# Performance work log

Hardware: AMD Instinct MI355X
Metric: run time of the kernel (lower is better)

The kernel has to match this reference:

```python
import jax, jax.numpy as jnp
import numpy as np

EPS = 1e-5


def setup_inputs() -> dict:
    key = jax.random.key(0)
    ks = jax.random.split(key, 12)
    B, C, H, W = 32, 512, 32, 32
    Ci = C // 2
    s_in = 1.0 / np.sqrt(C)
    s_ci = 1.0 / np.sqrt(Ci)
    return {
        "x": jax.random.normal(ks[0], (B, C, H, W), jnp.float32),
        # 1x1 conv weights stored as [out, in]
        "Wg": jax.random.normal(ks[1], (Ci, C), jnp.float32) * s_in,
        "bg": jax.random.normal(ks[2], (Ci,), jnp.float32) * 0.01,
        "Wt": jax.random.normal(ks[3], (Ci, C), jnp.float32) * s_in,
        "bt": jax.random.normal(ks[4], (Ci,), jnp.float32) * 0.01,
        "Wp": jax.random.normal(ks[5], (Ci, C), jnp.float32) * s_in,
        "bp": jax.random.normal(ks[6], (Ci,), jnp.float32) * 0.01,
        "Wz": jax.random.normal(ks[7], (C, Ci), jnp.float32) * s_ci,
        "bz": jax.random.normal(ks[8], (C,), jnp.float32) * 0.01,
        # BN affine params (torch inits these to 0 but we use nonzero for a meaningful baseline)
        "gamma": jax.random.normal(ks[9], (C,), jnp.float32) * 0.1,
        "beta": jax.random.normal(ks[10], (C,), jnp.float32) * 0.1,
    }


def reference(x, Wg, bg, Wt, bt, Wp, bp, Wz, bz, gamma, beta):
    B, C, H, W = x.shape
    N = H * W
    xr = x.reshape(B, C, N)
    # 1x1 conv projections (pure channel GEMMs)
    g_x = jnp.einsum('oc,bcn->bno', Wg, xr) + bg            # [B,N,Ci]
    theta_x = jnp.einsum('oc,bcn->bno', Wt, xr) + bt        # [B,N,Ci]
    phi_x = jnp.einsum('oc,bcn->bon', Wp, xr) + bp[None, :, None]  # [B,Ci,N]
    # full non-local attention over all N=H*W positions
    f = jnp.einsum('bnc,bcm->bnm', theta_x, phi_x)          # [B,N,N]
    attn = jax.nn.softmax(f, axis=-1)
    y = jnp.einsum('bnm,bmo->bon', attn, g_x)               # [B,Ci,N]
    # output 1x1 conv
    w_y = jnp.einsum('oc,bcn->bon', Wz, y) + bz[None, :, None]  # [B,C,N]
    # BatchNorm2d (training mode: batch statistics over B and spatial dims)
    mean = jnp.mean(w_y, axis=(0, 2), keepdims=True)
    var = jnp.var(w_y, axis=(0, 2), keepdims=True)
    w_y = (w_y - mean) / jnp.sqrt(var + EPS)
    w_y = w_y * gamma[None, :, None] + beta[None, :, None]
    return w_y.reshape(B, C, H, W) + x
```

## Files before the change

### kernel.cpp

```cpp
#include <hip/hip_runtime.h>
#include <math.h>

typedef __bf16 bf16;
typedef __bf16 bf16x8 __attribute__((ext_vector_type(8)));
typedef float f32x4 __attribute__((ext_vector_type(4)));
typedef unsigned short u16;
typedef unsigned int u32;

constexpr int BATCH = 32;
constexpr int CH    = 512;
constexpr int CI    = 256;
constexpr int NSP   = 1024;
constexpr int OCH   = 768;
constexpr float EPSV = 1e-5f;

__device__ __forceinline__ void gload_lds16(const bf16* g, bf16* l) {
    __builtin_amdgcn_global_load_lds(
        (const __attribute__((address_space(1))) void*)g,
        (__attribute__((address_space(3))) void*)l, 16, 0, 0);
}

__global__ void prep_weights(const float* __restrict__ Wg, const float* __restrict__ Wt,
                             const float* __restrict__ Wp, const float* __restrict__ Wz,
                             bf16* __restrict__ wc, bf16* __restrict__ wz,
                             float* __restrict__ sums) {
    int tid = blockIdx.x * 256 + threadIdx.x;
    if (tid < 1024) sums[tid] = 0.0f;
    if (tid < OCH * CH) {
        int r = tid / CH, c = tid % CH;
        float v;
        if (r < 256)      v = Wt[r * CH + c];
        else if (r < 512) v = Wp[(r - 256) * CH + c];
        else              v = Wg[(r - 512) * CH + c];
        wc[(size_t)(c >> 6) * (OCH * 64) + r * 64 + (c & 63)] = (bf16)v;
    } else {
        int t2 = tid - OCH * CH;
        if (t2 < CH * CI) {
            int r = t2 / CI, o = t2 % CI;
            wz[(size_t)(o >> 6) * (CH * 64) + r * 64 + (o & 63)] = (bf16)Wz[r * CI + o];
        }
    }
}

__global__ void transpose_x(const float* __restrict__ x, bf16* __restrict__ xb) {
    __shared__ bf16 tile[64][64];
    int b = blockIdx.z, kt = blockIdx.y, nb = blockIdx.x;
    int t = threadIdx.x;
    {
        int c_loc = t >> 2;
        int nq = t & 3;
        const float* src = x + ((size_t)b * CH + kt * 64 + c_loc) * NSP + nb * 64 + nq * 16;
        float vv[16];
        *(float4*)(vv + 0)  = *(const float4*)(src + 0);
        *(float4*)(vv + 4)  = *(const float4*)(src + 4);
        *(float4*)(vv + 8)  = *(const float4*)(src + 8);
        *(float4*)(vv + 12) = *(const float4*)(src + 12);
        int nbase = nq * 16;
        #pragma unroll
        for (int i = 0; i < 16; ++i) tile[nbase + i][c_loc] = (bf16)vv[i];
    }
    __syncthreads();
    {
        int n_loc = t >> 2;
        int cq = t & 3;
        bf16* dst = xb + ((((size_t)b * 8 + kt) * NSP) + nb * 64 + n_loc) * 64 + cq * 16;
        *(uint4*)(dst)     = *(const uint4*)&tile[n_loc][cq * 16];
        *(uint4*)(dst + 8) = *(const uint4*)&tile[n_loc][cq * 16 + 8];
    }
}

__launch_bounds__(256, 2)
__global__ void proj_gemm(const bf16* __restrict__ xb, const bf16* __restrict__ wc,
                          const float* __restrict__ bt, const float* __restrict__ bp,
                          const float* __restrict__ bg,
                          bf16* __restrict__ theta, bf16* __restrict__ phi_t,
                          bf16* __restrict__ gt_t) {
    constexpr int LDA = 72;
    __shared__ __align__(16) bf16 sm[2 * 128 * LDA];
    bf16* As = sm;
    bf16* Bs = sm + 128 * LDA;
    int b = blockIdx.z;
    int n0 = blockIdx.y * 128;
    int oc0 = blockIdx.x * 128;
    int t = threadIdx.x, lane = t & 63, wid = t >> 6;
    int wm = wid >> 1, wn = wid & 1;
    int l15 = lane & 15, quad = lane >> 4;

    f32x4 acc[4][4] = {};
    for (int kt = 0; kt < 8; ++kt) {
        __syncthreads();
        const bf16* asrc = xb + ((((size_t)b * 8 + kt) * NSP) + n0) * 64;
        const bf16* bsrc = wc + ((size_t)kt * OCH + oc0) * 64;
        for (int s = t; s < 1024; s += 256) {
            int row = s >> 3, c8 = s & 7;
            *(uint4*)&As[row * LDA + c8 * 8] = *(const uint4*)(asrc + (size_t)s * 8);
            *(uint4*)&Bs[row * LDA + c8 * 8] = *(const uint4*)(bsrc + (size_t)s * 8);
        }
        __syncthreads();
        #pragma unroll
        for (int kc = 0; kc < 2; ++kc) {
            bf16x8 af[4], bfv[4];
            #pragma unroll
            for (int i = 0; i < 4; ++i) {
                af[i]  = *(const bf16x8*)&As[(wm * 64 + i * 16 + l15) * LDA + kc * 32 + quad * 8];
                bfv[i] = *(const bf16x8*)&Bs[(wn * 64 + i * 16 + l15) * LDA + kc * 32 + quad * 8];
            }
            #pragma unroll
            for (int i = 0; i < 4; ++i)
                #pragma unroll
                for (int j = 0; j < 4; ++j)
                    acc[i][j] = __builtin_amdgcn_mfma_f32_16x16x32_bf16(af[i], bfv[j], acc[i][j], 0, 0, 0);
        }
    }
    if (oc0 < 256) {
        #pragma unroll
        for (int j = 0; j < 4; ++j) {
            int och = oc0 + wn * 64 + j * 16 + l15;
            float bv = bt[och];
            #pragma unroll
            for (int i = 0; i < 4; ++i) {
                int nrow = n0 + wm * 64 + i * 16 + quad * 4;
                bf16* p = theta + ((size_t)b * NSP + nrow) * CI + och;
                #pragma unroll
                for (int r = 0; r < 4; ++r)
                    p[(size_t)r * CI] = (bf16)(acc[i][j][r] + bv);
            }
        }
    } else if (oc0 < 512) {
        bf16* dstb = phi_t + (size_t)b * 262144;
        #pragma unroll
        for (int j = 0; j < 4; ++j) {
            int och = (oc0 - 256) + wn * 64 + j * 16 + l15;
            float bv = bp[och];
            int kc = och >> 5, qd = (och >> 3) & 3, e = och & 7;
            #pragma unroll
            for (int i = 0; i < 4; ++i) {
                int nrow = n0 + wm * 64 + i * 16 + quad * 4;
                int kt = nrow >> 5, h = (nrow >> 4) & 1;
                bf16* p = dstb + (size_t)kt * 8192 +
                          (size_t)(((h * 8 + kc) * 64 + qd * 16 + quad * 4) * 8) + e;
                #pragma unroll
                for (int r = 0; r < 4; ++r)
                    p[r * 8] = (bf16)(acc[i][j][r] + bv);
            }
        }
    } else {
        constexpr int LT = 136;
        int obase = oc0 - 512;
        __syncthreads();
        bf16* T = sm;
        #pragma unroll
        for (int j = 0; j < 4; ++j) {
            int och = wn * 64 + j * 16 + l15;
            float bv = bg[obase + och];
            #pragma unroll
            for (int i = 0; i < 4; ++i) {
                int nl = wm * 64 + i * 16 + quad * 4;
                bf16 tmp[4];
                #pragma unroll
                for (int r = 0; r < 4; ++r) tmp[r] = (bf16)(acc[i][j][r] + bv);
                *(uint2*)&T[och * LT + nl] = *(const uint2*)tmp;
            }
        }
        __syncthreads();
        bf16* dstb = gt_t + (size_t)b * 262144;
        for (int s = t; s < 2048; s += 256) {
            int row = s >> 4, part = s & 15;
            int o = obase + row;
            int kglob = n0 + part * 8;
            int kt = kglob >> 5, qd = (kglob >> 3) & 3;
            *(uint4*)(dstb + (size_t)kt * 8192 +
                      (size_t)(((o >> 4) * 64 + qd * 16 + (o & 15)) * 8)) =
                *(const uint4*)&T[row * LT + part * 8];
        }
    }
}

__launch_bounds__(256, 2)
__global__ void attn_kernel(const bf16* __restrict__ theta, const bf16* __restrict__ phi_t,
                            const bf16* __restrict__ gt_t, bf16* __restrict__ y) {
    constexpr int LP = 40;
    __shared__ __align__(16) char smem[70656];
    bf16* Pw = (bf16*)(smem + 65536);

    int id = blockIdx.x;
    int j = id >> 3;
    int qt = j & 15;
    int b = (id & 7) + 8 * (j >> 4);

    int t = threadIdx.x, lane = t & 63, w = t >> 6;
    int l15 = lane & 15, quad = lane >> 4;

    const bf16* ph_b = phi_t + (size_t)b * 262144 + w * 2048 + lane * 8;
    const bf16* gt_b = gt_t + (size_t)b * 262144 + w * 2048 + lane * 8;

    bf16x8 qf[8];
    {
        const bf16* qrow = theta + ((size_t)b * NSP + qt * 64 + w * 16 + l15) * CI;
        #pragma unroll
        for (int kc = 0; kc < 8; ++kc)
            qf[kc] = *(const bf16x8*)(qrow + kc * 32 + quad * 8);
    }

    {
        bf16* kdst = (bf16*)(smem)         + w * 2048;
        bf16* vdst = (bf16*)(smem + 32768) + w * 2048;
        #pragma unroll
        for (int i = 0; i < 4; ++i) {
            gload_lds16(ph_b + i * 512, kdst + i * 512);
            gload_lds16(gt_b + i * 512, vdst + i * 512);
        }
    }
    __syncthreads();

    f32x4 oacc[16] = {};
    float m[4] = {-1e30f, -1e30f, -1e30f, -1e30f};
    float ps[4] = {0.f, 0.f, 0.f, 0.f};

    for (int kt = 0; kt < 32; ++kt) {
        int cur = kt & 1;
        bf16* Kc = (bf16*)(smem + (cur << 14));
        bf16* Vc = (bf16*)(smem + 32768 + (cur << 14));

        if (kt < 31) {
            const bf16* ksrc = ph_b + (size_t)(kt + 1) * 8192;
            const bf16* vsrc = gt_b + (size_t)(kt + 1) * 8192;
            bf16* kdst = (bf16*)(smem + ((1 - cur) << 14)) + w * 2048;
            bf16* vdst = (bf16*)(smem + 32768 + ((1 - cur) << 14)) + w * 2048;
            #pragma unroll
            for (int i = 0; i < 4; ++i) {
                gload_lds16(ksrc + i * 512, kdst + i * 512);
                gload_lds16(vsrc + i * 512, vdst + i * 512);
            }
        }

        f32x4 s0 = {}, s1 = {};
        __builtin_amdgcn_s_setprio(1);
        #pragma unroll
        for (int kc = 0; kc < 8; ++kc) {
            bf16x8 kf0 = *(const bf16x8*)(Kc + kc * 512 + lane * 8);
            bf16x8 kf1 = *(const bf16x8*)(Kc + 4096 + kc * 512 + lane * 8);
            s0 = __builtin_amdgcn_mfma_f32_16x16x32_bf16(qf[kc], kf0, s0, 0, 0, 0);
            s1 = __builtin_amdgcn_mfma_f32_16x16x32_bf16(qf[kc], kf1, s1, 0, 0, 0);
        }
        __builtin_amdgcn_s_setprio(0);

        float cmx[4]; int flag = 0;
        #pragma unroll
        for (int r = 0; r < 4; ++r) {
            float c = fmaxf(s0[r], s1[r]);
            c = fmaxf(c, __shfl_xor(c, 1));
            c = fmaxf(c, __shfl_xor(c, 2));
            c = fmaxf(c, __shfl_xor(c, 4));
            c = fmaxf(c, __shfl_xor(c, 8));
            cmx[r] = c;
            flag |= (c > m[r] + 8.0f) ? 1 : 0;
        }
        if (__any(flag)) {
            float alpha[4];
            #pragma unroll
            for (int r = 0; r < 4; ++r) {
                float mn = fmaxf(m[r], cmx[r]);
                alpha[r] = __expf(m[r] - mn);
                m[r] = mn;
                ps[r] *= alpha[r];
            }
            #pragma unroll
            for (int nt = 0; nt < 16; ++nt) {
                oacc[nt][0] *= alpha[0];
                oacc[nt][1] *= alpha[1];
                oacc[nt][2] *= alpha[2];
                oacc[nt][3] *= alpha[3];
            }
        }
        #pragma unroll
        for (int r = 0; r < 4; ++r) {
            float p0 = __expf(s0[r] - m[r]);
            float p1 = __expf(s1[r] - m[r]);
            ps[r] += p0 + p1;
            Pw[(w * 16 + quad * 4 + r) * LP + l15]      = (bf16)p0;
            Pw[(w * 16 + quad * 4 + r) * LP + 16 + l15] = (bf16)p1;
        }

        bf16x8 pf = *(const bf16x8*)&Pw[(w * 16 + l15) * LP + quad * 8];
        __builtin_amdgcn_s_setprio(1);
        #pragma unroll
        for (int nt = 0; nt < 16; ++nt) {
            bf16x8 vf = *(const bf16x8*)(Vc + nt * 512 + lane * 8);
            oacc[nt] = __builtin_amdgcn_mfma_f32_16x16x32_bf16(pf, vf, oacc[nt], 0, 0, 0);
        }
        __builtin_amdgcn_s_setprio(0);

        __syncthreads();
    }

    #pragma unroll
    for (int r = 0; r < 4; ++r) {
        ps[r] += __shfl_xor(ps[r], 1);
        ps[r] += __shfl_xor(ps[r], 2);
        ps[r] += __shfl_xor(ps[r], 4);
        ps[r] += __shfl_xor(ps[r], 8);
    }
    float inv[4];
    #pragma unroll
    for (int r = 0; r < 4; ++r) inv[r] = 1.0f / ps[r];

    int nrow = qt * 64 + w * 16 + quad * 4;
    #pragma unroll
    for (int nt = 0; nt < 16; ++nt) {
        int o = nt * 16 + l15;
        bf16* dst = y + ((((size_t)b * 4 + (o >> 6)) * NSP) + nrow) * 64 + (o & 63);
        #pragma unroll
        for (int r = 0; r < 4; ++r)
            dst[(size_t)r * 64] = (bf16)(oacc[nt][r] * inv[r]);
    }
}

__launch_bounds__(256, 4)
__global__ void out_gemm(const bf16* __restrict__ y, const bf16* __restrict__ wz,
                         const float* __restrict__ bz, float* __restrict__ wy,
                         float* __restrict__ sums) {
    constexpr int LDA = 72;
    __shared__ __align__(16) bf16 As[128 * LDA];
    __shared__ __align__(16) bf16 Bs[128 * LDA];
    __shared__ float redS[128][2], redS2[128][2];
    int b = blockIdx.z;
    int co0 = blockIdx.y * 128;
    int n0 = blockIdx.x * 128;
    int t = threadIdx.x, lane = t & 63, wid = t >> 6;
    int wm = wid >> 1, wn = wid & 1;
    int l15 = lane & 15, quad = lane >> 4;

    f32x4 acc[4][4] = {};
    for (int kt = 0; kt < 4; ++kt) {
        __syncthreads();
        const bf16* asrc = wz + ((size_t)kt * CH + co0) * 64;
        const bf16* bsrc = y + ((((size_t)b * 4 + kt) * NSP) + n0) * 64;
        for (int s = t; s < 1024; s += 256) {
            int row = s >> 3, c8 = s & 7;
            *(uint4*)&As[row * LDA + c8 * 8] = *(const uint4*)(asrc + (size_t)s * 8);
            *(uint4*)&Bs[row * LDA + c8 * 8] = *(const uint4*)(bsrc + (size_t)s * 8);
        }
        __syncthreads();
        #pragma unroll
        for (int kc = 0; kc < 2; ++kc) {
            bf16x8 af[4], bfv[4];
            #pragma unroll
            for (int i = 0; i < 4; ++i) {
                af[i]  = *(const bf16x8*)&As[(wm * 64 + i * 16 + l15) * LDA + kc * 32 + quad * 8];
                bfv[i] = *(const bf16x8*)&Bs[(wn * 64 + i * 16 + l15) * LDA + kc * 32 + quad * 8];
            }
            #pragma unroll
            for (int i = 0; i < 4; ++i)
                #pragma unroll
                for (int j = 0; j < 4; ++j)
                    acc[i][j] = __builtin_amdgcn_mfma_f32_16x16x32_bf16(af[i], bfv[j], acc[i][j], 0, 0, 0);
        }
    }
    #pragma unroll
    for (int i = 0; i < 4; ++i) {
        int cbase = co0 + wm * 64 + i * 16 + quad * 4;
        #pragma unroll
        for (int r = 0; r < 4; ++r) {
            int c = cbase + r;
            float bv = bz[c];
            float s = 0.f, s2 = 0.f;
            #pragma unroll
            for (int jj = 0; jj < 4; ++jj) {
                int n = n0 + wn * 64 + jj * 16 + l15;
                float v = acc[i][jj][r] + bv;
                wy[((size_t)b * CH + c) * NSP + n] = v;
                s += v; s2 += v * v;
            }
            s  += __shfl_xor(s, 1);  s2 += __shfl_xor(s2, 1);
            s  += __shfl_xor(s, 2);  s2 += __shfl_xor(s2, 2);
            s  += __shfl_xor(s, 4);  s2 += __shfl_xor(s2, 4);
            s  += __shfl_xor(s, 8);  s2 += __shfl_xor(s2, 8);
            if (l15 == 0) {
                int cl = wm * 64 + i * 16 + quad * 4 + r;
                redS[cl][wn]  = s;
                redS2[cl][wn] = s2;
            }
        }
    }
    __syncthreads();
    if (t < 128) {
        atomicAdd(&sums[co0 + t],      redS[t][0] + redS[t][1]);
        atomicAdd(&sums[CH + co0 + t], redS2[t][0] + redS2[t][1]);
    }
}

__global__ void bn_finalize(float* __restrict__ out, const float* __restrict__ x,
                            const float* __restrict__ sums,
                            const float* __restrict__ gamma, const float* __restrict__ beta) {
    size_t idx4 = (size_t)blockIdx.x * 256 + threadIdx.x;
    size_t flat = idx4 * 4;
    int ch = (int)((flat >> 10) & 511);
    float S = sums[ch], S2 = sums[CH + ch];
    const float invcnt = 1.0f / (BATCH * NSP);
    float mean = S * invcnt;
    float var = S2 * invcnt - mean * mean;
    float sc = rsqrtf(var + EPSV) * gamma[ch];
    float bi = beta[ch] - mean * sc;
    float4 wv = *(float4*)(out + flat);
    float4 xv = *(const float4*)(x + flat);
    wv.x = wv.x * sc + bi + xv.x;
    wv.y = wv.y * sc + bi + xv.y;
    wv.z = wv.z * sc + bi + xv.z;
    wv.w = wv.w * sc + bi + xv.w;
    *(float4*)(out + flat) = wv;
}

extern "C" void kernel_launch(void* const* d_in, const int* in_sizes, int n_in,
                              void* d_out, int out_size, void* d_ws, size_t ws_size,
                              hipStream_t stream) {
    const float* x     = (const float*)d_in[0];
    const float* Wg    = (const float*)d_in[1];
    const float* bg    = (const float*)d_in[2];
    const float* Wt    = (const float*)d_in[3];
    const float* bt    = (const float*)d_in[4];
    const float* Wp    = (const float*)d_in[5];
    const float* bp    = (const float*)d_in[6];
    const float* Wz    = (const float*)d_in[7];
    const float* bz    = (const float*)d_in[8];
    const float* gamma = (const float*)d_in[9];
    const float* beta  = (const float*)d_in[10];
    float* out = (float*)d_out;

    char* ws = (char*)d_ws;
    bf16*  y_t   = (bf16*)(ws);
    bf16*  g_t   = (bf16*)(ws + 16777216);
    bf16*  wc    = (bf16*)(ws + 33554432);
    bf16*  wzb   = (bf16*)(ws + 34340864);
    float* sums  = (float*)(ws + 34603008);

    char* ob = (char*)d_out;
    bf16* xb    = (bf16*)(ob);
    bf16* theta = (bf16*)(ob + 33554432);
    bf16* phi_t = (bf16*)(ob + 50331648);

    prep_weights<<<dim3(2048), dim3(256), 0, stream>>>(Wg, Wt, Wp, Wz, wc, wzb, sums);
    transpose_x<<<dim3(16, 8, 32), dim3(256), 0, stream>>>(x, xb);
    proj_gemm<<<dim3(6, 8, 32), dim3(256), 0, stream>>>(xb, wc, bt, bp, bg, theta, phi_t, g_t);
    attn_kernel<<<dim3(512), dim3(256), 0, stream>>>(theta, phi_t, g_t, y_t);
    out_gemm<<<dim3(8, 4, 32), dim3(256), 0, stream>>>(y_t, wzb, bz, out, sums);
    bn_finalize<<<dim3(16384), dim3(256), 0, stream>>>(out, x, sums, gamma, beta);
}
```

Before: 299.7 us.

## Process two 16-row query tiles per warp in attention kernel

Each warp now handles 32 query rows instead of 16, so every K and V fragment read from LDS feeds two MFMAs. The launch uses half as many blocks (256), each covering 128 query rows. This cuts LDS and global K/V traffic per query, but doubles accumulator registers, drops the occupancy hint to 1 block per CU, and leaves only 256 blocks, which may underfill a 256-CU device.

```diff
diff --git a/kernel.cpp b/kernel.cpp
--- a/kernel.cpp
+++ b/kernel.cpp
@@ -176,17 +176,16 @@
     }
 }
 
-__launch_bounds__(256, 2)
+__launch_bounds__(256, 1)
 __global__ void attn_kernel(const bf16* __restrict__ theta, const bf16* __restrict__ phi_t,
                             const bf16* __restrict__ gt_t, bf16* __restrict__ y) {
     constexpr int LP = 40;
-    __shared__ __align__(16) char smem[70656];
+    __shared__ __align__(16) char smem[75776];
     bf16* Pw = (bf16*)(smem + 65536);
 
     int id = blockIdx.x;
-    int j = id >> 3;
-    int qt = j & 15;
-    int b = (id & 7) + 8 * (j >> 4);
+    int b = (id & 7) + 8 * (id >> 6);
+    int qt = (id >> 3) & 7;
 
     int t = threadIdx.x, lane = t & 63, w = t >> 6;
     int l15 = lane & 15, quad = lane >> 4;
@@ -194,12 +193,13 @@
     const bf16* ph_b = phi_t + (size_t)b * 262144 + w * 2048 + lane * 8;
     const bf16* gt_b = gt_t + (size_t)b * 262144 + w * 2048 + lane * 8;
 
-    bf16x8 qf[8];
-    {
-        const bf16* qrow = theta + ((size_t)b * NSP + qt * 64 + w * 16 + l15) * CI;
+    bf16x8 qf[2][8];
+    #pragma unroll
+    for (int i = 0; i < 2; ++i) {
+        const bf16* qrow = theta + ((size_t)b * NSP + qt * 128 + w * 32 + i * 16 + l15) * CI;
         #pragma unroll
         for (int kc = 0; kc < 8; ++kc)
-            qf[kc] = *(const bf16x8*)(qrow + kc * 32 + quad * 8);
+            qf[i][kc] = *(const bf16x8*)(qrow + kc * 32 + quad * 8);
     }
 
     {
@@ -213,9 +213,9 @@
     }
     __syncthreads();
 
-    f32x4 oacc[16] = {};
-    float m[4] = {-1e30f, -1e30f, -1e30f, -1e30f};
-    float ps[4] = {0.f, 0.f, 0.f, 0.f};
+    f32x4 oacc[2][16] = {};
+    float m[2][4]  = {{-1e30f, -1e30f, -1e30f, -1e30f}, {-1e30f, -1e30f, -1e30f, -1e30f}};
+    float ps[2][4] = {{0.f, 0.f, 0.f, 0.f}, {0.f, 0.f, 0.f, 0.f}};
 
     for (int kt = 0; kt < 32; ++kt) {
         int cur = kt & 1;
@@ -234,60 +234,73 @@
             }
         }
 
-        f32x4 s0 = {}, s1 = {};
+        f32x4 s[2][2] = {};
         __builtin_amdgcn_s_setprio(1);
         #pragma unroll
         for (int kc = 0; kc < 8; ++kc) {
             bf16x8 kf0 = *(const bf16x8*)(Kc + kc * 512 + lane * 8);
             bf16x8 kf1 = *(const bf16x8*)(Kc + 4096 + kc * 512 + lane * 8);
-            s0 = __builtin_amdgcn_mfma_f32_16x16x32_bf16(qf[kc], kf0, s0, 0, 0, 0);
-            s1 = __builtin_amdgcn_mfma_f32_16x16x32_bf16(qf[kc], kf1, s1, 0, 0, 0);
+            s[0][0] = __builtin_amdgcn_mfma_f32_16x16x32_bf16(qf[0][kc], kf0, s[0][0], 0, 0, 0);
+            s[1][0] = __builtin_amdgcn_mfma_f32_16x16x32_bf16(qf[1][kc], kf0, s[1][0], 0, 0, 0);
+            s[0][1] = __builtin_amdgcn_mfma_f32_16x16x32_bf16(qf[0][kc], kf1, s[0][1], 0, 0, 0);
+            s[1][1] = __builtin_amdgcn_mfma_f32_16x16x32_bf16(qf[1][kc], kf1, s[1][1], 0, 0, 0);
         }
         __builtin_amdgcn_s_setprio(0);
 
-        float cmx[4]; int flag = 0;
-        #pragma unroll
-        for (int r = 0; r < 4; ++r) {
-            float c = fmaxf(s0[r], s1[r]);
-            c = fmaxf(c, __shfl_xor(c, 1));
-            c = fmaxf(c, __shfl_xor(c, 2));
-            c = fmaxf(c, __shfl_xor(c, 4));
-            c = fmaxf(c, __shfl_xor(c, 8));
-            cmx[r] = c;
-            flag |= (c > m[r] + 8.0f) ? 1 : 0;
+        float cmx[2][4]; int flag = 0;
+        #pragma unroll
+        for (int i = 0; i < 2; ++i) {
+            #pragma unroll
+            for (int r = 0; r < 4; ++r) {
+                float c = fmaxf(s[i][0][r], s[i][1][r]);
+                c = fmaxf(c, __shfl_xor(c, 1));
+                c = fmaxf(c, __shfl_xor(c, 2));
+                c = fmaxf(c, __shfl_xor(c, 4));
+                c = fmaxf(c, __shfl_xor(c, 8));
+                cmx[i][r] = c;
+                flag |= (c > m[i][r] + 8.0f) ? 1 : 0;
+            }
         }
         if (__any(flag)) {
-            float alpha[4];
+            #pragma unroll
+            for (int i = 0; i < 2; ++i) {
+                float alpha[4];
+                #pragma unroll
+                for (int r = 0; r < 4; ++r) {
+                    float mn = fmaxf(m[i][r], cmx[i][r]);
+                    alpha[r] = __expf(m[i][r] - mn);
+                    m[i][r] = mn;
+                    ps[i][r] *= alpha[r];
+                }
+                #pragma unroll
+                for (int nt = 0; nt < 16; ++nt) {
+                    oacc[i][nt][0] *= alpha[0];
+                    oacc[i][nt][1] *= alpha[1];
+                    oacc[i][nt][2] *= alpha[2];
+                    oacc[i][nt][3] *= alpha[3];
+                }
+            }
+        }
+        #pragma unroll
+        for (int i = 0; i < 2; ++i) {
             #pragma unroll
             for (int r = 0; r < 4; ++r) {
-                float mn = fmaxf(m[r], cmx[r]);
-                alpha[r] = __expf(m[r] - mn);
-                m[r] = mn;
-                ps[r] *= alpha[r];
-            }
-            #pragma unroll
-            for (int nt = 0; nt < 16; ++nt) {
-                oacc[nt][0] *= alpha[0];
-                oacc[nt][1] *= alpha[1];
-                oacc[nt][2] *= alpha[2];
-                oacc[nt][3] *= alpha[3];
-            }
-        }
-        #pragma unroll
-        for (int r = 0; r < 4; ++r) {
-            float p0 = __expf(s0[r] - m[r]);
-            float p1 = __expf(s1[r] - m[r]);
-            ps[r] += p0 + p1;
-            Pw[(w * 16 + quad * 4 + r) * LP + l15]      = (bf16)p0;
-            Pw[(w * 16 + quad * 4 + r) * LP + 16 + l15] = (bf16)p1;
-        }
-
-        bf16x8 pf = *(const bf16x8*)&Pw[(w * 16 + l15) * LP + quad * 8];
+                float p0 = __expf(s[i][0][r] - m[i][r]);
+                float p1 = __expf(s[i][1][r] - m[i][r]);
+                ps[i][r] += p0 + p1;
+                Pw[(w * 32 + i * 16 + quad * 4 + r) * LP + l15]      = (bf16)p0;
+                Pw[(w * 32 + i * 16 + quad * 4 + r) * LP + 16 + l15] = (bf16)p1;
+            }
+        }
+
+        bf16x8 pf0 = *(const bf16x8*)&Pw[(w * 32 + l15) * LP + quad * 8];
+        bf16x8 pf1 = *(const bf16x8*)&Pw[(w * 32 + 16 + l15) * LP + quad * 8];
         __builtin_amdgcn_s_setprio(1);
         #pragma unroll
         for (int nt = 0; nt < 16; ++nt) {
             bf16x8 vf = *(const bf16x8*)(Vc + nt * 512 + lane * 8);
-            oacc[nt] = __builtin_amdgcn_mfma_f32_16x16x32_bf16(pf, vf, oacc[nt], 0, 0, 0);
+            oacc[0][nt] = __builtin_amdgcn_mfma_f32_16x16x32_bf16(pf0, vf, oacc[0][nt], 0, 0, 0);
+            oacc[1][nt] = __builtin_amdgcn_mfma_f32_16x16x32_bf16(pf1, vf, oacc[1][nt], 0, 0, 0);
         }
         __builtin_amdgcn_s_setprio(0);
 
@@ -295,24 +308,30 @@
     }
 
     #pragma unroll
-    for (int r = 0; r < 4; ++r) {
-        ps[r] += __shfl_xor(ps[r], 1);
-        ps[r] += __shfl_xor(ps[r], 2);
-        ps[r] += __shfl_xor(ps[r], 4);
-        ps[r] += __shfl_xor(ps[r], 8);
-    }
-    float inv[4];
+    for (int i = 0; i < 2; ++i) {
+        #pragma unroll
+        for (int r = 0; r < 4; ++r) {
+            ps[i][r] += __shfl_xor(ps[i][r], 1);
+            ps[i][r] += __shfl_xor(ps[i][r], 2);
+            ps[i][r] += __shfl_xor(ps[i][r], 4);
+            ps[i][r] += __shfl_xor(ps[i][r], 8);
+        }
+    }
+
     #pragma unroll
-    for (int r = 0; r < 4; ++r) inv[r] = 1.0f / ps[r];
-
-    int nrow = qt * 64 + w * 16 + quad * 4;
-    #pragma unroll
-    for (int nt = 0; nt < 16; ++nt) {
-        int o = nt * 16 + l15;
-        bf16* dst = y + ((((size_t)b * 4 + (o >> 6)) * NSP) + nrow) * 64 + (o & 63);
-        #pragma unroll
-        for (int r = 0; r < 4; ++r)
-            dst[(size_t)r * 64] = (bf16)(oacc[nt][r] * inv[r]);
+    for (int i = 0; i < 2; ++i) {
+        float inv[4];
+        #pragma unroll
+        for (int r = 0; r < 4; ++r) inv[r] = 1.0f / ps[i][r];
+        int nrow = qt * 128 + w * 32 + i * 16 + quad * 4;
+        #pragma unroll
+        for (int nt = 0; nt < 16; ++nt) {
+            int o = nt * 16 + l15;
+            bf16* dst = y + ((((size_t)b * 4 + (o >> 6)) * NSP) + nrow) * 64 + (o & 63);
+            #pragma unroll
+            for (int r = 0; r < 4; ++r)
+                dst[(size_t)r * 64] = (bf16)(oacc[i][nt][r] * inv[r]);
+        }
     }
 }
 
@@ -442,7 +461,7 @@
     prep_weights<<<dim3(2048), dim3(256), 0, stream>>>(Wg, Wt, Wp, Wz, wc, wzb, sums);
     transpose_x<<<dim3(16, 8, 32), dim3(256), 0, stream>>>(x, xb);
     proj_gemm<<<dim3(6, 8, 32), dim3(256), 0, stream>>>(xb, wc, bt, bp, bg, theta, phi_t, g_t);
-    attn_kernel<<<dim3(512), dim3(256), 0, stream>>>(theta, phi_t, g_t, y_t);
+    attn_kernel<<<dim3(256), dim3(256), 0, stream>>>(theta, phi_t, g_t, y_t);
     out_gemm<<<dim3(8, 4, 32), dim3(256), 0, stream>>>(y_t, wzb, bz, out, sums);
     bn_finalize<<<dim3(16384), dim3(256), 0, stream>>>(out, x, sums, gamma, beta);
 }
```

New measurement: 334.7 us. +11.7%, slower.

## Compute transposed scores to keep P in registers, skip LDS round-trip

Applied to the files above, without the earlier changes.

The QK^T MFMA now takes K as the A operand and Q as the B operand, so each lane holds score values for one query row across keys. Those probabilities are packed directly into the bf16x8 operand for the PV MFMA, which removes the shared-memory store, reload and staging buffer. The V (g) layout written by the projection kernel is permuted to match the new key ordering. Row max and row sum now need only two cross-lane shuffles, but the rescale factors and final normalisers must be broadcast back with extra shuffles.

```diff
diff --git a/kernel.cpp b/kernel.cpp
--- a/kernel.cpp
+++ b/kernel.cpp
@@ -18,6 +18,12 @@
     __builtin_amdgcn_global_load_lds(
         (const __attribute__((address_space(1))) void*)g,
         (__attribute__((address_space(3))) void*)l, 16, 0, 0);
+}
+
+__device__ __forceinline__ u32 pack_bf16(float a, float b) {
+    union { bf16 h; u16 u; } ca, cb;
+    ca.h = (bf16)a; cb.h = (bf16)b;
+    return (u32)ca.u | ((u32)cb.u << 16);
 }
 
 __global__ void prep_weights(const float* __restrict__ Wg, const float* __restrict__ Wt,
@@ -169,9 +175,11 @@
             int o = obase + row;
             int kglob = n0 + part * 8;
             int kt = kglob >> 5, qd = (kglob >> 3) & 3;
-            *(uint4*)(dstb + (size_t)kt * 8192 +
-                      (size_t)(((o >> 4) * 64 + qd * 16 + (o & 15)) * 8)) =
-                *(const uint4*)&T[row * LT + part * 8];
+            int qa = (2 * qd) & 3, qb = (2 * qd + 1) & 3;
+            int jb = (qd & 2) * 2;
+            bf16* base = dstb + (size_t)kt * 8192 + (size_t)((o >> 4) * 512 + (o & 15) * 8);
+            *(uint2*)(base + qa * 128 + jb) = *(const uint2*)&T[row * LT + part * 8];
+            *(uint2*)(base + qb * 128 + jb) = *(const uint2*)&T[row * LT + part * 8 + 4];
         }
     }
 }
@@ -179,9 +187,7 @@
 __launch_bounds__(256, 2)
 __global__ void attn_kernel(const bf16* __restrict__ theta, const bf16* __restrict__ phi_t,
                             const bf16* __restrict__ gt_t, bf16* __restrict__ y) {
-    constexpr int LP = 40;
-    __shared__ __align__(16) char smem[70656];
-    bf16* Pw = (bf16*)(smem + 65536);
+    __shared__ __align__(16) char smem[65536];
 
     int id = blockIdx.x;
     int j = id >> 3;
@@ -214,8 +220,8 @@
     __syncthreads();
 
     f32x4 oacc[16] = {};
-    float m[4] = {-1e30f, -1e30f, -1e30f, -1e30f};
-    float ps[4] = {0.f, 0.f, 0.f, 0.f};
+    float m = -1e30f;
+    float ps = 0.0f;
 
     for (int kt = 0; kt < 32; ++kt) {
         int cur = kt & 1;
@@ -240,49 +246,49 @@
         for (int kc = 0; kc < 8; ++kc) {
             bf16x8 kf0 = *(const bf16x8*)(Kc + kc * 512 + lane * 8);
             bf16x8 kf1 = *(const bf16x8*)(Kc + 4096 + kc * 512 + lane * 8);
-            s0 = __builtin_amdgcn_mfma_f32_16x16x32_bf16(qf[kc], kf0, s0, 0, 0, 0);
-            s1 = __builtin_amdgcn_mfma_f32_16x16x32_bf16(qf[kc], kf1, s1, 0, 0, 0);
+            s0 = __builtin_amdgcn_mfma_f32_16x16x32_bf16(kf0, qf[kc], s0, 0, 0, 0);
+            s1 = __builtin_amdgcn_mfma_f32_16x16x32_bf16(kf1, qf[kc], s1, 0, 0, 0);
         }
         __builtin_amdgcn_s_setprio(0);
 
-        float cmx[4]; int flag = 0;
-        #pragma unroll
-        for (int r = 0; r < 4; ++r) {
-            float c = fmaxf(s0[r], s1[r]);
-            c = fmaxf(c, __shfl_xor(c, 1));
-            c = fmaxf(c, __shfl_xor(c, 2));
-            c = fmaxf(c, __shfl_xor(c, 4));
-            c = fmaxf(c, __shfl_xor(c, 8));
-            cmx[r] = c;
-            flag |= (c > m[r] + 8.0f) ? 1 : 0;
-        }
+        float c = fmaxf(fmaxf(fmaxf(s0[0], s0[1]), fmaxf(s0[2], s0[3])),
+                        fmaxf(fmaxf(s1[0], s1[1]), fmaxf(s1[2], s1[3])));
+        c = fmaxf(c, __shfl_xor(c, 16));
+        c = fmaxf(c, __shfl_xor(c, 32));
+        int flag = (c > m + 8.0f) ? 1 : 0;
         if (__any(flag)) {
-            float alpha[4];
-            #pragma unroll
-            for (int r = 0; r < 4; ++r) {
-                float mn = fmaxf(m[r], cmx[r]);
-                alpha[r] = __expf(m[r] - mn);
-                m[r] = mn;
-                ps[r] *= alpha[r];
-            }
+            float mn = fmaxf(m, c);
+            float alpha = __expf(m - mn);
+            m = mn;
+            ps *= alpha;
+            float a0 = __shfl(alpha, quad * 4 + 0);
+            float a1 = __shfl(alpha, quad * 4 + 1);
+            float a2 = __shfl(alpha, quad * 4 + 2);
+            float a3 = __shfl(alpha, quad * 4 + 3);
             #pragma unroll
             for (int nt = 0; nt < 16; ++nt) {
-                oacc[nt][0] *= alpha[0];
-                oacc[nt][1] *= alpha[1];
-                oacc[nt][2] *= alpha[2];
-                oacc[nt][3] *= alpha[3];
-            }
-        }
-        #pragma unroll
-        for (int r = 0; r < 4; ++r) {
-            float p0 = __expf(s0[r] - m[r]);
-            float p1 = __expf(s1[r] - m[r]);
-            ps[r] += p0 + p1;
-            Pw[(w * 16 + quad * 4 + r) * LP + l15]      = (bf16)p0;
-            Pw[(w * 16 + quad * 4 + r) * LP + 16 + l15] = (bf16)p1;
-        }
-
-        bf16x8 pf = *(const bf16x8*)&Pw[(w * 16 + l15) * LP + quad * 8];
+                oacc[nt][0] *= a0;
+                oacc[nt][1] *= a1;
+                oacc[nt][2] *= a2;
+                oacc[nt][3] *= a3;
+            }
+        }
+        float p0 = __expf(s0[0] - m), p1 = __expf(s0[1] - m);
+        float p2 = __expf(s0[2] - m), p3 = __expf(s0[3] - m);
+        float p4 = __expf(s1[0] - m), p5 = __expf(s1[1] - m);
+        float p6 = __expf(s1[2] - m), p7 = __expf(s1[3] - m);
+        ps += ((p0 + p1) + (p2 + p3)) + ((p4 + p5) + (p6 + p7));
+
+        bf16x8 pf;
+        {
+            union { u32 u[4]; bf16x8 v; } cvt;
+            cvt.u[0] = pack_bf16(p0, p1);
+            cvt.u[1] = pack_bf16(p2, p3);
+            cvt.u[2] = pack_bf16(p4, p5);
+            cvt.u[3] = pack_bf16(p6, p7);
+            pf = cvt.v;
+        }
+
         __builtin_amdgcn_s_setprio(1);
         #pragma unroll
         for (int nt = 0; nt < 16; ++nt) {
@@ -294,25 +300,23 @@
         __syncthreads();
     }
 
-    #pragma unroll
-    for (int r = 0; r < 4; ++r) {
-        ps[r] += __shfl_xor(ps[r], 1);
-        ps[r] += __shfl_xor(ps[r], 2);
-        ps[r] += __shfl_xor(ps[r], 4);
-        ps[r] += __shfl_xor(ps[r], 8);
-    }
-    float inv[4];
-    #pragma unroll
-    for (int r = 0; r < 4; ++r) inv[r] = 1.0f / ps[r];
+    ps += __shfl_xor(ps, 16);
+    ps += __shfl_xor(ps, 32);
+    float inv = 1.0f / ps;
+    float inv0 = __shfl(inv, quad * 4 + 0);
+    float inv1 = __shfl(inv, quad * 4 + 1);
+    float inv2 = __shfl(inv, quad * 4 + 2);
+    float inv3 = __shfl(inv, quad * 4 + 3);
 
     int nrow = qt * 64 + w * 16 + quad * 4;
     #pragma unroll
     for (int nt = 0; nt < 16; ++nt) {
         int o = nt * 16 + l15;
         bf16* dst = y + ((((size_t)b * 4 + (o >> 6)) * NSP) + nrow) * 64 + (o & 63);
-        #pragma unroll
-        for (int r = 0; r < 4; ++r)
-            dst[(size_t)r * 64] = (bf16)(oacc[nt][r] * inv[r]);
+        dst[0]           = (bf16)(oacc[nt][0] * inv0);
+        dst[(size_t)64]  = (bf16)(oacc[nt][1] * inv1);
+        dst[(size_t)128] = (bf16)(oacc[nt][2] * inv2);
+        dst[(size_t)192] = (bf16)(oacc[nt][3] * inv3);
     }
 }
 
```

Result: faster. 289.8 us (-3.3%).
